# Optimization experiments

Measured on AMD Instinct MI355X. Metric: run time of the kernel, lower is better.

Reference implementation:

```python
import jax, jax.numpy as jnp
import numpy as np

HEADS = 16
DIM_HEAD = 64
SCALE = DIM_HEAD ** -0.5
EPS = 1e-5


def _bitlinear(x, w):
    """BitNet b1.58 BitLinear (kyegomez/BitNet), eval-mode, bias-free.
    w: [out, in] torch-layout. Ternary weight quant (scale = mean|w|),
    per-token int8 absmax activation quant, straight-through estimator.
    """
    ws = 1.0 / jnp.clip(jnp.mean(jnp.abs(w)), EPS, None)
    wq = jnp.clip(jnp.round(w * ws), -1.0, 1.0) / ws
    wq = w + jax.lax.stop_gradient(wq - w)
    xs = 127.0 / jnp.clip(jnp.max(jnp.abs(x), axis=-1, keepdims=True), EPS, None)
    xq = jnp.clip(jnp.round(x * xs), -128.0, 127.0) / xs
    xq = x + jax.lax.stop_gradient(xq - x)
    return jnp.einsum('bnd,od->bno', xq, wq)


def setup_inputs() -> dict:
    key = jax.random.key(0)
    ks = jax.random.split(key, 6)
    b, n, d = 2, 2048, 1024
    return {
        'x': jax.random.normal(ks[0], (b, n, d), dtype=jnp.float32),
        'context': jax.random.normal(ks[1], (b, n, d), dtype=jnp.float32),
        'Wq': jax.random.normal(ks[2], (d, d), dtype=jnp.float32) * 0.02,
        'Wk': jax.random.normal(ks[3], (d, d), dtype=jnp.float32) * 0.02,
        'Wv': jax.random.normal(ks[4], (d, d), dtype=jnp.float32) * 0.02,
        'Wo': jax.random.normal(ks[5], (d, d), dtype=jnp.float32) * 0.02,
    }


def reference(x, context, Wq, Wk, Wv, Wo):
    b, n, _ = x.shape
    m = context.shape[1]
    q = _bitlinear(x, Wq)
    k = _bitlinear(context, Wk)
    v = _bitlinear(context, Wv)
    # b n (h d) -> b h n d
    q = q.reshape(b, n, HEADS, DIM_HEAD).transpose(0, 2, 1, 3)
    k = k.reshape(b, m, HEADS, DIM_HEAD).transpose(0, 2, 1, 3)
    v = v.reshape(b, m, HEADS, DIM_HEAD).transpose(0, 2, 1, 3)
    dots = jnp.einsum('bhid,bhjd->bhij', q, k) * SCALE
    attn = jax.nn.softmax(dots, axis=-1)  # dropout is identity in eval
    out = jnp.einsum('bhij,bhjd->bhid', attn, v)
    out = out.transpose(0, 2, 1, 3).reshape(b, n, HEADS * DIM_HEAD)
    return _bitlinear(out, Wo)
```

## Files before the change

### kernel.cpp

```cpp
#include <hip/hip_runtime.h>
#include <math.h>

#define HEADS   16
#define DHEAD   64
#define SEQ     2048
#define NB      2
#define DM      1024
#define NTOK    4096
#define WEPS    1e-5

using f16x8   = __attribute__((ext_vector_type(8))) _Float16;
using f16x4   = __attribute__((ext_vector_type(4))) _Float16;
using floatx4 = __attribute__((ext_vector_type(4))) float;
using i32x4   = __attribute__((ext_vector_type(4))) int;

typedef __attribute__((address_space(1))) unsigned int gu32;
typedef __attribute__((address_space(3))) unsigned int lu32;

#define BAR_LGKM()  asm volatile("s_waitcnt lgkmcnt(0)\n\ts_barrier" ::: "memory")
#define WAIT_LGKM() asm volatile("s_waitcnt lgkmcnt(0)" ::: "memory")

__device__ __forceinline__ unsigned short h16b(_Float16 h) {
    union { _Float16 h; unsigned short u; } c; c.h = h; return c.u;
}

__global__ void wsum1(const float* __restrict__ w0, const float* __restrict__ w1,
                      const float* __restrict__ w2, const float* __restrict__ w3,
                      double* __restrict__ partial) {
    const float* w = (blockIdx.y == 0) ? w0 : (blockIdx.y == 1) ? w1 : (blockIdx.y == 2) ? w2 : w3;
    int base = blockIdx.x * 16384;
    double s = 0.0;
    for (int i = threadIdx.x; i < 16384; i += 256)
        s += fabs((double)w[base + i]);
    __shared__ double sd[256];
    sd[threadIdx.x] = s;
    __syncthreads();
    for (int st = 128; st > 0; st >>= 1) {
        if (threadIdx.x < st) sd[threadIdx.x] += sd[threadIdx.x + st];
        __syncthreads();
    }
    if (threadIdx.x == 0) partial[blockIdx.y * 64 + blockIdx.x] = sd[0];
}

__global__ void wsum2(const double* __restrict__ partial, double* __restrict__ wscale) {
    int t = threadIdx.x;
    if (t < 4) {
        double s = 0.0;
        for (int i = 0; i < 64; i++) s += partial[t * 64 + i];
        double mean = s / (1024.0 * 1024.0);
        wscale[t] = (mean > WEPS) ? mean : WEPS;
    }
}

__global__ void wquant(const float* __restrict__ w0, const float* __restrict__ w1,
                       const float* __restrict__ w2, const float* __restrict__ w3,
                       const double* __restrict__ wscale, signed char* __restrict__ wq) {
    int widx = blockIdx.y;
    const float* w = (widx == 0) ? w0 : (widx == 1) ? w1 : (widx == 2) ? w2 : w3;
    double ws = 1.0 / wscale[widx];
    int idx = (blockIdx.x * 256 + threadIdx.x) * 4;
    float4 wv = *(const float4*)(w + idx);
    char4 o;
    {
        double r = rint((double)wv.x * ws); r = r > 1.0 ? 1.0 : (r < -1.0 ? -1.0 : r); o.x = (signed char)r;
    } {
        double r = rint((double)wv.y * ws); r = r > 1.0 ? 1.0 : (r < -1.0 ? -1.0 : r); o.y = (signed char)r;
    } {
        double r = rint((double)wv.z * ws); r = r > 1.0 ? 1.0 : (r < -1.0 ? -1.0 : r); o.z = (signed char)r;
    } {
        double r = rint((double)wv.w * ws); r = r > 1.0 ? 1.0 : (r < -1.0 ? -1.0 : r); o.w = (signed char)r;
    }
    *(char4*)(wq + (size_t)widx * 1048576 + idx) = o;
}

__device__ __forceinline__ void aquant_row(const float* __restrict__ row,
                                           signed char* __restrict__ dst_row,
                                           double* __restrict__ ascale_p) {
    int t = threadIdx.x;
    float4 xv = *(const float4*)(row + t * 4);
    float a = fmaxf(fmaxf(fabsf(xv.x), fabsf(xv.y)), fmaxf(fabsf(xv.z), fabsf(xv.w)));
    __shared__ float sm[256];
    sm[t] = a;
    __syncthreads();
    for (int st = 128; st > 0; st >>= 1) {
        if (t < st) sm[t] = fmaxf(sm[t], sm[t + st]);
        __syncthreads();
    }
    double mx = (double)sm[0];
    if (mx < WEPS) mx = WEPS;
    if (t == 0) *ascale_p = mx / 127.0;
    double xs = 127.0 / mx;
    char4 o;
    {
        double r = rint((double)xv.x * xs); r = r > 127.0 ? 127.0 : (r < -128.0 ? -128.0 : r); o.x = (signed char)r;
    } {
        double r = rint((double)xv.y * xs); r = r > 127.0 ? 127.0 : (r < -128.0 ? -128.0 : r); o.y = (signed char)r;
    } {
        double r = rint((double)xv.z * xs); r = r > 127.0 ? 127.0 : (r < -128.0 ? -128.0 : r); o.z = (signed char)r;
    } {
        double r = rint((double)xv.w * xs); r = r > 127.0 ? 127.0 : (r < -128.0 ? -128.0 : r); o.w = (signed char)r;
    }
    *(char4*)(dst_row + t * 4) = o;
}

__global__ void aquant(const float* __restrict__ src, signed char* __restrict__ dst,
                       double* __restrict__ ascale) {
    int tok = blockIdx.x;
    aquant_row(src + (size_t)tok * DM, dst + (size_t)tok * DM, ascale + tok);
}

__global__ void aquant2(const float* __restrict__ x, const float* __restrict__ ctx,
                        signed char* __restrict__ dst, double* __restrict__ ascale) {
    int tok = blockIdx.x;
    const float* row = (tok < NTOK) ? x + (size_t)tok * DM : ctx + (size_t)(tok - NTOK) * DM;
    aquant_row(row, dst + (size_t)tok * DM, ascale + tok);
}

__device__ __forceinline__ void gemm_core(
        const signed char* __restrict__ A, const signed char* __restrict__ W,
        const double* __restrict__ ascale, double wsc,
        void* __restrict__ outp, int mode, float prescale, int bx, int by) {
    __shared__ __align__(16) signed char lds_a[128 * 64];
    __shared__ __align__(16) signed char lds_b[128 * 64];
    const int tid  = threadIdx.x;
    const int wave = tid >> 6, lane = tid & 63;
    const int wr = wave >> 1, wc = wave & 1;
    const int quad = lane >> 4, l15 = lane & 15;
    const int row0 = by * 128, col0 = bx * 128;
    i32x4 acc[4][4] = {};

    const signed char* ga0 = A + (size_t)(row0 + (lane >> 2)) * DM + (lane & 3) * 16;
    const signed char* gb0 = W + (size_t)(col0 + (lane >> 2)) * DM + (lane & 3) * 16;

    for (int k0 = 0; k0 < DM; k0 += 64) {
        __syncthreads();
        #pragma unroll
        for (int t = 0; t < 2; t++) {
            const int i = wave + t * 4;
            __builtin_amdgcn_global_load_lds(
                (const gu32*)(const void*)(ga0 + (size_t)i * 16 * DM + k0),
                (lu32*)(void*)(lds_a + i * 1024), 16, 0, 0);
            __builtin_amdgcn_global_load_lds(
                (const gu32*)(const void*)(gb0 + (size_t)i * 16 * DM + k0),
                (lu32*)(void*)(lds_b + i * 1024), 16, 0, 0);
        }
        __syncthreads();
        i32x4 af[4], bfr[4];
        #pragma unroll
        for (int mi = 0; mi < 4; mi++) {
            int r = wr * 64 + mi * 16 + l15;
            af[mi] = *(const i32x4*)&lds_a[r * 64 + quad * 16];
        }
        #pragma unroll
        for (int ni = 0; ni < 4; ni++) {
            int n = wc * 64 + ni * 16 + l15;
            bfr[ni] = *(const i32x4*)&lds_b[n * 64 + quad * 16];
        }
        #pragma unroll
        for (int mi = 0; mi < 4; mi++)
            #pragma unroll
            for (int ni = 0; ni < 4; ni++)
                acc[mi][ni] = __builtin_amdgcn_mfma_i32_16x16x64_i8(af[mi], bfr[ni], acc[mi][ni], 0, 0, 0);
    }

    #pragma unroll
    for (int mi = 0; mi < 4; mi++) {
        int tbase = row0 + wr * 64 + mi * 16 + quad * 4;
        #pragma unroll
        for (int reg = 0; reg < 4; reg++) {
            int t = tbase + reg;
            double sa = ascale[t] * wsc;
            #pragma unroll
            for (int ni = 0; ni < 4; ni++) {
                int o = col0 + wc * 64 + ni * 16 + l15;
                float val = (float)((double)acc[mi][ni][reg] * sa);
                if (mode == 1) {
                    ((float*)outp)[(size_t)t * DM + o] = val;
                } else {
                    int bb = t >> 11, n = t & 2047, hh = o >> 6, dh = o & 63;
                    float fv = val * prescale;
                    _Float16 hl = (_Float16)fv;
                    _Float16 ml = (_Float16)((fv - (float)hl) * 2048.0f);
                    if (mode == 0) {
                        size_t idx = (((size_t)(bb * HEADS + hh) * SEQ + n) << 6) + dh;
                        ((unsigned short*)outp)[idx]           = h16b(hl);
                        ((unsigned short*)outp)[idx + 4194304] = h16b(ml);
                    } else {
                        size_t idx = (((size_t)(bb * HEADS + hh) * 64 + dh) << 11) + n;
                        ((unsigned short*)outp)[idx]           = h16b(hl);
                        ((unsigned short*)outp)[idx + 4194304] = h16b(ml);
                    }
                }
            }
        }
    }
}

__global__ __launch_bounds__(256) void gemm_qkv(
        const signed char* __restrict__ xq, const signed char* __restrict__ cq,
        const signed char* __restrict__ wqb, const double* __restrict__ ascale_x,
        const double* __restrict__ wscale, void* __restrict__ qkv) {
    const int which = blockIdx.x >> 3;
    char* base = (char*)qkv + (size_t)which * 16777216;
    gemm_core(which == 0 ? xq : cq,
              wqb + (size_t)which * 1048576,
              ascale_x + (which ? NTOK : 0),
              wscale[which],
              base,
              which == 2 ? 2 : 0,
              which == 0 ? 0.18033688011112042f : 1.0f, blockIdx.x & 7, blockIdx.y);
}

__global__ __launch_bounds__(256) void gemm_o(
        const signed char* __restrict__ aq, const signed char* __restrict__ wo,
        const double* __restrict__ ascale, const double* __restrict__ wscale_p,
        float* __restrict__ out) {
    gemm_core(aq, wo, ascale, *wscale_p, out, 1, 1.0f, blockIdx.x, blockIdx.y);
}

#define KH_IDX(row, d8) (((row) * 8 + ((d8) ^ ((row) & 7))) * 8)
#define VSW(row) (((row) >> 1) & 3)

__global__ __launch_bounds__(256, 4) void attn_mfma(
        const unsigned short* __restrict__ qhg, const unsigned short* __restrict__ qlg,
        const unsigned short* __restrict__ khg, const unsigned short* __restrict__ klg,
        const unsigned short* __restrict__ vhg, const unsigned short* __restrict__ vlg,
        float* __restrict__ out) {
    __shared__ __align__(16) _Float16 KhL[32 * 64];
    __shared__ __align__(16) _Float16 KlL[32 * 64];
    __shared__ __align__(16) _Float16 VhL[64 * 32];
    __shared__ __align__(16) _Float16 VlL[64 * 32];
    __shared__ __align__(16) _Float16 PhL[4][16 * 36];
    __shared__ __align__(16) _Float16 PlL[4][16 * 36];
    __shared__ float Lp[4][16][4];

    const int lin  = blockIdx.x;
    const int bh   = (lin & 7) * 4 + (lin >> 8);
    const int qblk = (lin >> 3) & 31;
    const int tid  = threadIdx.x;
    const int wave = tid >> 6, lane = tid & 63;
    const int l15  = lane & 15, quad = lane >> 4;
    const int qbase = qblk * 64 + wave * 16;

    f16x8 qh[2], qm[2];
    #pragma unroll
    for (int c = 0; c < 2; c++) {
        size_t off = (((size_t)bh * SEQ + qbase + l15) << 6) + c * 32 + quad * 8;
        qh[c] = *(const f16x8*)(qhg + off);
        qm[c] = *(const f16x8*)(qlg + off);
    }

    floatx4 och[4] = {};
    floatx4 ocm[4] = {};
    float lsum = 0.f;

    const unsigned short* khb = khg + ((size_t)bh * SEQ << 6);
    const unsigned short* klb = klg + ((size_t)bh * SEQ << 6);
    const unsigned short* vhb = vhg + ((size_t)bh << 17);
    const unsigned short* vlb = vlg + ((size_t)bh << 17);

    const int kk = tid >> 3, d8 = tid & 7;
    const int vrow = tid >> 2, vc = tid & 3;
    const int vcs  = vc ^ VSW(vrow);
    const unsigned short* vsh = vhb + ((size_t)vrow << 11) + vc * 8;
    const unsigned short* vsl = vlb + ((size_t)vrow << 11) + vc * 8;

    uint4 kh_pf = *(const uint4*)(khb + ((size_t)kk << 6) + d8 * 8);
    uint4 kl_pf = *(const uint4*)(klb + ((size_t)kk << 6) + d8 * 8);
    uint4 vh_pf = *(const uint4*)(vsh);
    uint4 vl_pf = *(const uint4*)(vsl);

    for (int kt = 0; kt < SEQ; kt += 32) {
        BAR_LGKM();

        *(uint4*)&KhL[KH_IDX(kk, d8)] = kh_pf;
        *(uint4*)&KlL[KH_IDX(kk, d8)] = kl_pf;
        *(uint4*)&VhL[(vrow * 4 + vcs) * 8] = vh_pf;
        *(uint4*)&VlL[(vrow * 4 + vcs) * 8] = vl_pf;

        if (kt + 32 < SEQ) {
            kh_pf = *(const uint4*)(khb + ((size_t)(kt + 32 + kk) << 6) + d8 * 8);
            kl_pf = *(const uint4*)(klb + ((size_t)(kt + 32 + kk) << 6) + d8 * 8);
            vh_pf = *(const uint4*)(vsh + kt + 32);
            vl_pf = *(const uint4*)(vsl + kt + 32);
        }

        BAR_LGKM();

        f16x8 kfh[2][2], kfl[2][2];
        #pragma unroll
        for (int ms = 0; ms < 2; ms++) {
            #pragma unroll
            for (int c = 0; c < 2; c++) {
                kfh[ms][c] = *(const f16x8*)&KhL[KH_IDX(ms * 16 + l15, c * 4 + quad)];
                kfl[ms][c] = *(const f16x8*)&KlL[KH_IDX(ms * 16 + l15, c * 4 + quad)];
            }
        }

        #pragma unroll
        for (int ms = 0; ms < 2; ms++) {
            floatx4 ah = {}, am = {};
            #pragma unroll
            for (int c = 0; c < 2; c++) {
                ah = __builtin_amdgcn_mfma_f32_16x16x32_f16(kfh[ms][c], qh[c], ah, 0, 0, 0);
                am = __builtin_amdgcn_mfma_f32_16x16x32_f16(kfh[ms][c], qm[c], am, 0, 0, 0);
                am = __builtin_amdgcn_mfma_f32_16x16x32_f16(kfl[ms][c], qh[c], am, 0, 0, 0);
            }
            float p[4];
            #pragma unroll
            for (int r = 0; r < 4; r++) {
                float s = ah[r] + am[r] * 4.8828125e-4f;
                p[r] = exp2f(s);
                lsum += p[r];
            }
            f16x4 hv, lv;
            #pragma unroll
            for (int r = 0; r < 4; r++) {
                _Float16 h = (_Float16)p[r];
                hv[r] = h;
                lv[r] = (_Float16)((p[r] - (float)h) * 2048.0f);
            }
            int poff = l15 * 36 + ms * 16 + quad * 4;
            *(f16x4*)&PhL[wave][poff] = hv;
            *(f16x4*)&PlL[wave][poff] = lv;
        }
        WAIT_LGKM();

        f16x8 pfh = *(const f16x8*)&PhL[wave][l15 * 36 + quad * 8];
        f16x8 pfm = *(const f16x8*)&PlL[wave][l15 * 36 + quad * 8];
        #pragma unroll
        for (int nh = 0; nh < 4; nh++) {
            int vro = nh * 16 + l15;
            int vof = (vro * 4 + (quad ^ VSW(vro))) * 8;
            f16x8 vfh = *(const f16x8*)&VhL[vof];
            f16x8 vfm = *(const f16x8*)&VlL[vof];
            och[nh] = __builtin_amdgcn_mfma_f32_16x16x32_f16(pfh, vfh, och[nh], 0, 0, 0);
            ocm[nh] = __builtin_amdgcn_mfma_f32_16x16x32_f16(pfh, vfm, ocm[nh], 0, 0, 0);
            ocm[nh] = __builtin_amdgcn_mfma_f32_16x16x32_f16(pfm, vfh, ocm[nh], 0, 0, 0);
        }
    }

    Lp[wave][l15][quad] = lsum;
    WAIT_LGKM();

    int b = bh >> 4, h = bh & 15;
    float linv[4];
    #pragma unroll
    for (int r = 0; r < 4; r++) {
        float4 lv = *(const float4*)&Lp[wave][quad * 4 + r][0];
        linv[r] = 1.0f / (lv.x + lv.y + lv.z + lv.w);
    }
    #pragma unroll
    for (int nh = 0; nh < 4; nh++) {
        #pragma unroll
        for (int r = 0; r < 4; r++) {
            int token = b * SEQ + qbase + quad * 4 + r;
            float val = (och[nh][r] + ocm[nh][r] * 4.8828125e-4f) * linv[r];
            out[(size_t)token * DM + h * 64 + nh * 16 + l15] = val;
        }
    }
}

extern "C" void kernel_launch(void* const* d_in, const int* in_sizes, int n_in,
                              void* d_out, int out_size, void* d_ws, size_t ws_size,
                              hipStream_t stream) {
    const float* x       = (const float*)d_in[0];
    const float* context = (const float*)d_in[1];
    const float* Wq      = (const float*)d_in[2];
    const float* Wk      = (const float*)d_in[3];
    const float* Wv      = (const float*)d_in[4];
    const float* Wo      = (const float*)d_in[5];
    char* ws = (char*)d_ws;

    double* wscale   = (double*)(ws + 0);
    double* partial  = (double*)(ws + 4096);
    double* ascale_x = (double*)(ws + 8192);
    double* ascale_a = (double*)(ws + 73728);
    signed char* wqb = (signed char*)(ws + 131072);
    signed char* xq  = (signed char*)(ws + 4325376);
    signed char* cq  = (signed char*)(ws + 8519680);
    float* attn_out  = (float*)(ws + 4325376);
    char* planes     = ws + 21102592;
    signed char* aq  = (signed char*)(ws + 21102592);

    unsigned short* qhg = (unsigned short*)planes;
    unsigned short* qlg = qhg + 4194304;
    unsigned short* khg = (unsigned short*)(planes + 16777216);
    unsigned short* klg = khg + 4194304;
    unsigned short* vhg = (unsigned short*)(planes + 33554432);
    unsigned short* vlg = vhg + 4194304;

    wsum1<<<dim3(64, 4), 256, 0, stream>>>(Wq, Wk, Wv, Wo, partial);
    wsum2<<<1, 64, 0, stream>>>(partial, wscale);
    wquant<<<dim3(1024, 4), 256, 0, stream>>>(Wq, Wk, Wv, Wo, wscale, wqb);
    aquant2<<<2 * NTOK, 256, 0, stream>>>(x, context, xq, ascale_x);

    gemm_qkv<<<dim3(24, 32), 256, 0, stream>>>(xq, cq, wqb, ascale_x, wscale, planes);

    attn_mfma<<<dim3(1024), 256, 0, stream>>>(qhg, qlg, khg, klg, vhg, vlg, attn_out);

    aquant<<<NTOK, 256, 0, stream>>>(attn_out, aq, ascale_a);
    gemm_o<<<dim3(8, 32), 256, 0, stream>>>(aq, wqb + 3145728, ascale_a, wscale + 3, (float*)d_out);
}
```

Before: 317.8 us.

## Vectorize transposed V stores and streamline attention softmax with packed conversions and setprio

The mode-2 epilogue of the GEMM, which writes V transposed, now packs four consecutive tokens into ushort4 stores instead of scalar 16-bit stores. The attention inner loop issues all QK MFMAs for both sub-tiles before the exp step, uses the hardware exp2 builtin and packed round-to-zero f16 conversion, and brackets MFMA blocks with s_setprio. The goal is fewer memory transactions and fewer VALU instructions on the softmax path. Round-to-zero conversion changes the hi/lo split rounding slightly, though the lo term still captures the residual.

Measured after the change: 294.1 us. 1.08x faster.

```diff
diff --git a/kernel.cpp b/kernel.cpp
--- a/kernel.cpp
+++ b/kernel.cpp
@@ -11,6 +11,7 @@
 
 using f16x8   = __attribute__((ext_vector_type(8))) _Float16;
 using f16x4   = __attribute__((ext_vector_type(4))) _Float16;
+using fp16x2  = __attribute__((ext_vector_type(2))) __fp16;
 using floatx4 = __attribute__((ext_vector_type(4))) float;
 using i32x4   = __attribute__((ext_vector_type(4))) int;
 
@@ -22,6 +23,9 @@
 
 __device__ __forceinline__ unsigned short h16b(_Float16 h) {
     union { _Float16 h; unsigned short u; } c; c.h = h; return c.u;
+}
+__device__ __forceinline__ unsigned pk2u(fp16x2 v) {
+    union { fp16x2 h; unsigned u; } c; c.h = v; return c.u;
 }
 
 __global__ void wsum1(const float* __restrict__ w0, const float* __restrict__ w1,
@@ -166,27 +170,43 @@
     #pragma unroll
     for (int mi = 0; mi < 4; mi++) {
         int tbase = row0 + wr * 64 + mi * 16 + quad * 4;
-        #pragma unroll
-        for (int reg = 0; reg < 4; reg++) {
-            int t = tbase + reg;
-            double sa = ascale[t] * wsc;
+        if (mode == 2) {
+            int bb = tbase >> 11, n = tbase & 2047;
             #pragma unroll
             for (int ni = 0; ni < 4; ni++) {
                 int o = col0 + wc * 64 + ni * 16 + l15;
-                float val = (float)((double)acc[mi][ni][reg] * sa);
-                if (mode == 1) {
-                    ((float*)outp)[(size_t)t * DM + o] = val;
-                } else {
-                    int bb = t >> 11, n = t & 2047, hh = o >> 6, dh = o & 63;
-                    float fv = val * prescale;
+                int hh = o >> 6, dh = o & 63;
+                ushort4 hv, lv;
+                #pragma unroll
+                for (int reg = 0; reg < 4; reg++) {
+                    double sa = ascale[tbase + reg] * wsc;
+                    float fv = (float)((double)acc[mi][ni][reg] * sa) * prescale;
                     _Float16 hl = (_Float16)fv;
                     _Float16 ml = (_Float16)((fv - (float)hl) * 2048.0f);
-                    if (mode == 0) {
+                    ((unsigned short*)&hv)[reg] = h16b(hl);
+                    ((unsigned short*)&lv)[reg] = h16b(ml);
+                }
+                size_t idx = (((size_t)(bb * HEADS + hh) * 64 + dh) << 11) + n;
+                *(ushort4*)((unsigned short*)outp + idx)           = hv;
+                *(ushort4*)((unsigned short*)outp + idx + 4194304) = lv;
+            }
+        } else {
+            #pragma unroll
+            for (int reg = 0; reg < 4; reg++) {
+                int t = tbase + reg;
+                double sa = ascale[t] * wsc;
+                #pragma unroll
+                for (int ni = 0; ni < 4; ni++) {
+                    int o = col0 + wc * 64 + ni * 16 + l15;
+                    float val = (float)((double)acc[mi][ni][reg] * sa);
+                    if (mode == 1) {
+                        ((float*)outp)[(size_t)t * DM + o] = val;
+                    } else {
+                        int bb = t >> 11, n = t & 2047, hh = o >> 6, dh = o & 63;
+                        float fv = val * prescale;
+                        _Float16 hl = (_Float16)fv;
+                        _Float16 ml = (_Float16)((fv - (float)hl) * 2048.0f);
                         size_t idx = (((size_t)(bb * HEADS + hh) * SEQ + n) << 6) + dh;
-                        ((unsigned short*)outp)[idx]           = h16b(hl);
-                        ((unsigned short*)outp)[idx + 4194304] = h16b(ml);
-                    } else {
-                        size_t idx = (((size_t)(bb * HEADS + hh) * 64 + dh) << 11) + n;
                         ((unsigned short*)outp)[idx]           = h16b(hl);
                         ((unsigned short*)outp)[idx + 4194304] = h16b(ml);
                     }
@@ -253,6 +273,7 @@
     floatx4 och[4] = {};
     floatx4 ocm[4] = {};
     float lsum = 0.f;
+    const floatx4 zf = {};
 
     const unsigned short* khb = khg + ((size_t)bh * SEQ << 6);
     const unsigned short* klb = klg + ((size_t)bh * SEQ << 6);
@@ -297,37 +318,41 @@
             }
         }
 
+        __builtin_amdgcn_s_setprio(1);
+        floatx4 ah[2], am[2];
         #pragma unroll
         for (int ms = 0; ms < 2; ms++) {
-            floatx4 ah = {}, am = {};
-            #pragma unroll
-            for (int c = 0; c < 2; c++) {
-                ah = __builtin_amdgcn_mfma_f32_16x16x32_f16(kfh[ms][c], qh[c], ah, 0, 0, 0);
-                am = __builtin_amdgcn_mfma_f32_16x16x32_f16(kfh[ms][c], qm[c], am, 0, 0, 0);
-                am = __builtin_amdgcn_mfma_f32_16x16x32_f16(kfl[ms][c], qh[c], am, 0, 0, 0);
-            }
-            float p[4];
-            #pragma unroll
-            for (int r = 0; r < 4; r++) {
-                float s = ah[r] + am[r] * 4.8828125e-4f;
-                p[r] = exp2f(s);
-                lsum += p[r];
-            }
-            f16x4 hv, lv;
-            #pragma unroll
-            for (int r = 0; r < 4; r++) {
-                _Float16 h = (_Float16)p[r];
-                hv[r] = h;
-                lv[r] = (_Float16)((p[r] - (float)h) * 2048.0f);
-            }
+            ah[ms] = __builtin_amdgcn_mfma_f32_16x16x32_f16(kfh[ms][0], qh[0], zf, 0, 0, 0);
+            am[ms] = __builtin_amdgcn_mfma_f32_16x16x32_f16(kfh[ms][0], qm[0], zf, 0, 0, 0);
+            am[ms] = __builtin_amdgcn_mfma_f32_16x16x32_f16(kfl[ms][0], qh[0], am[ms], 0, 0, 0);
+            ah[ms] = __builtin_amdgcn_mfma_f32_16x16x32_f16(kfh[ms][1], qh[1], ah[ms], 0, 0, 0);
+            am[ms] = __builtin_amdgcn_mfma_f32_16x16x32_f16(kfh[ms][1], qm[1], am[ms], 0, 0, 0);
+            am[ms] = __builtin_amdgcn_mfma_f32_16x16x32_f16(kfl[ms][1], qh[1], am[ms], 0, 0, 0);
+        }
+        __builtin_amdgcn_s_setprio(0);
+
+        #pragma unroll
+        for (int ms = 0; ms < 2; ms++) {
+            float p0 = __builtin_amdgcn_exp2f(ah[ms][0] + am[ms][0] * 4.8828125e-4f);
+            float p1 = __builtin_amdgcn_exp2f(ah[ms][1] + am[ms][1] * 4.8828125e-4f);
+            float p2 = __builtin_amdgcn_exp2f(ah[ms][2] + am[ms][2] * 4.8828125e-4f);
+            float p3 = __builtin_amdgcn_exp2f(ah[ms][3] + am[ms][3] * 4.8828125e-4f);
+            lsum += (p0 + p1) + (p2 + p3);
+            fp16x2 h01 = __builtin_amdgcn_cvt_pkrtz(p0, p1);
+            fp16x2 h23 = __builtin_amdgcn_cvt_pkrtz(p2, p3);
+            fp16x2 m01 = __builtin_amdgcn_cvt_pkrtz((p0 - (float)h01[0]) * 2048.0f,
+                                                    (p1 - (float)h01[1]) * 2048.0f);
+            fp16x2 m23 = __builtin_amdgcn_cvt_pkrtz((p2 - (float)h23[0]) * 2048.0f,
+                                                    (p3 - (float)h23[1]) * 2048.0f);
             int poff = l15 * 36 + ms * 16 + quad * 4;
-            *(f16x4*)&PhL[wave][poff] = hv;
-            *(f16x4*)&PlL[wave][poff] = lv;
+            *(uint2*)&PhL[wave][poff] = make_uint2(pk2u(h01), pk2u(h23));
+            *(uint2*)&PlL[wave][poff] = make_uint2(pk2u(m01), pk2u(m23));
         }
         WAIT_LGKM();
 
         f16x8 pfh = *(const f16x8*)&PhL[wave][l15 * 36 + quad * 8];
         f16x8 pfm = *(const f16x8*)&PlL[wave][l15 * 36 + quad * 8];
+        __builtin_amdgcn_s_setprio(1);
         #pragma unroll
         for (int nh = 0; nh < 4; nh++) {
             int vro = nh * 16 + l15;
@@ -338,6 +363,7 @@
             ocm[nh] = __builtin_amdgcn_mfma_f32_16x16x32_f16(pfh, vfm, ocm[nh], 0, 0, 0);
             ocm[nh] = __builtin_amdgcn_mfma_f32_16x16x32_f16(pfm, vfh, ocm[nh], 0, 0, 0);
         }
+        __builtin_amdgcn_s_setprio(0);
     }
 
     Lp[wave][l15][quad] = lsum;
```
